# Performance work log

Measured on AMD Instinct MI355X. Metric: run time of the kernel, lower is better.

## Reference

```python
import jax, jax.numpy as jnp
import numpy as np

F, H, NSEQ, T, A, LP, LV = 256, 256, 64, 2048, 32, 512, 512
N = NSEQ * T


def setup_inputs() -> dict:
    key = jax.random.key(0)
    ks = jax.random.split(key, 24)
    p = lambda k, shape: jax.random.normal(k, shape, jnp.float32) * 0.05
    return {
        'features': jax.random.normal(ks[0], (N, F), jnp.float32),
        'episode_starts': (jax.random.uniform(ks[1], (N,)) < 0.005).astype(jnp.float32),
        'h_pi': jax.random.normal(ks[2], (1, NSEQ, H), jnp.float32),
        'c_pi': jax.random.normal(ks[3], (1, NSEQ, H), jnp.float32),
        'h_vf': jax.random.normal(ks[4], (1, NSEQ, H), jnp.float32),
        'c_vf': jax.random.normal(ks[5], (1, NSEQ, H), jnp.float32),
        'W_feat': p(ks[6], (4 * F, F)), 'b_feat': jnp.zeros((4 * F,), jnp.float32),
        'W_emb': p(ks[7], (H, F)), 'b_emb': jnp.zeros((H,), jnp.float32),
        'W_ih': p(ks[8], (4 * H, F)), 'W_hh': p(ks[9], (4 * H, H)),
        'b_ih': jnp.zeros((4 * H,), jnp.float32), 'b_hh': jnp.zeros((4 * H,), jnp.float32),
        'Wp1': p(ks[10], (LP, H + 3 * F)), 'bp1': jnp.zeros((LP,), jnp.float32),
        'Wp2': p(ks[11], (A, LP)), 'bp2': jnp.zeros((A,), jnp.float32),
        'Wv1': p(ks[12], (LV, H + 3 * F)), 'bv1': jnp.zeros((LV,), jnp.float32),
        'Wv2': p(ks[13], (1, LV)), 'bv2': jnp.zeros((1,), jnp.float32),
    }


def _lstm_masked_scan(feats, starts, h0, c0, W_ih, W_hh, b_ih, b_hh):
    # feats: (T, n_seq, F), starts: (T, n_seq); PyTorch gate order i,f,g,o
    xg = jnp.einsum('tnf,gf->tng', feats, W_ih) + b_ih  # precompute input gates

    def step(carry, xs):
        h, c = carry
        xg_t, s_t = xs
        m = (1.0 - s_t)[:, None]          # episode-reset mask
        h = h * m
        c = c * m
        g = xg_t + h @ W_hh.T + b_hh
        i, f, gg, o = jnp.split(g, 4, axis=-1)
        c = jax.nn.sigmoid(f) * c + jax.nn.sigmoid(i) * jnp.tanh(gg)
        h = jax.nn.sigmoid(o) * jnp.tanh(c)
        return (h, c), h

    (hT, cT), hs = jax.lax.scan(step, (h0, c0), (xg, starts))
    return hs, hT, cT


def reference(features, episode_starts, h_pi, c_pi, h_vf, c_vf,
              W_feat, b_feat, W_emb, b_emb, W_ih, W_hh, b_ih, b_hh,
              Wp1, bp1, Wp2, bp2, Wv1, bv1, Wv2, bv2):
    n_seq = h_vf.shape[1]
    feats = features.reshape(n_seq, -1, F).swapaxes(0, 1)      # (T, n_seq, F)
    starts = episode_starts.reshape(n_seq, -1).swapaxes(0, 1)  # (T, n_seq)

    feat4 = jnp.einsum('tnf,gf->tng', feats, W_feat) + b_feat  # (T, n_seq, 4F)
    f1 = feat4[..., : 3 * F]
    f1_flat = f1.swapaxes(0, 1).reshape(-1, 3 * F)             # (N, 3F)

    # actor branch: TempLSTM ignores its LSTM -> just Linear(F, H) on raw feats;
    # the loop branch feeds raw features_sequence (source behavior).
    out_pi = jnp.einsum('tnf,hf->tnh', feats, W_emb) + b_emb   # (T, n_seq, H)
    out_pi_flat = out_pi.swapaxes(0, 1).reshape(-1, H)

    # critic branch: masked LSTM recurrence with per-step episode resets
    hs, hT, cT = _lstm_masked_scan(feats, starts, h_vf[0], c_vf[0], W_ih, W_hh, b_ih, b_hh)
    hs_flat = hs.swapaxes(0, 1).reshape(-1, H)

    latent_pi = jnp.concatenate([f1_flat, out_pi_flat], axis=-1)
    latent_vf = jnp.concatenate([f1_flat, hs_flat], axis=-1)

    values = jax.nn.relu(latent_vf @ Wv1.T + bv1) @ Wv2.T + bv2      # (N, 1)
    logits = jax.nn.relu(latent_pi @ Wp1.T + bp1) @ Wp2.T + bp2      # (N, A)

    actions = jnp.argmax(logits, axis=-1)  # deterministic=True -> mode
    log_prob = jnp.take_along_axis(jax.nn.log_softmax(logits, axis=-1), actions[:, None], axis=1)[:, 0]

    # actor final state = h0 scaled by product of reset masks (loop semantics)
    mprod = jnp.prod(1.0 - starts, axis=0)[None, :, None]
    h_pi_f, c_pi_f = h_pi * mprod, c_pi * mprod
    return actions, values, log_prob, h_pi_f, c_pi_f, hT[None], cT[None]
```

## Files before the change

### kernel.cpp

```cpp
#include <hip/hip_runtime.h>
#include <stdint.h>
#include <math.h>

#define N_TOT 131072
#define TSEQ  2048
#define NSEQ  64
#define CS    128
#define NCH   16
#define PARTS 4

typedef unsigned long long u64;

__global__ __launch_bounds__(256)
void transpose_whh(const float* __restrict__ Whh, float* __restrict__ Wg)
{
    const int k = blockIdx.x;
    const int u = threadIdx.x;
#pragma unroll
    for (int g = 0; g < 4; ++g)
        Wg[(size_t)k * 1024 + u * 4 + g] = Whh[(size_t)(g * 256 + u) * 256 + k];
}

__global__ __launch_bounds__(256)
void gemm_xg(const float* __restrict__ A, const float* __restrict__ Wih,
             const float* __restrict__ bih, const float* __restrict__ bhh,
             float* __restrict__ xg, int base)
{
    __shared__ float As[16][136];
    __shared__ float Bs[16][136];
    const int t  = threadIdx.x;
    const int n0 = blockIdx.x * 128;
    const int seq = blockIdx.y;
    const size_t grow0 = (size_t)seq * TSEQ + base;
    const size_t lrow0 = (size_t)seq * CS;
    const int tx = t & 15, ty = t >> 4;

    float acc[8][8];
#pragma unroll
    for (int i = 0; i < 8; ++i)
#pragma unroll
        for (int j = 0; j < 8; ++j) acc[i][j] = 0.f;

    for (int kt = 0; kt < 256; kt += 16) {
#pragma unroll
        for (int jj = 0; jj < 2; ++jj) {
            int idx = t + 256 * jj;
            int m = idx >> 2, q = idx & 3;
            float4 a = *(const float4*)(A + (grow0 + m) * 256 + kt + q * 4);
            As[q * 4 + 0][m] = a.x; As[q * 4 + 1][m] = a.y;
            As[q * 4 + 2][m] = a.z; As[q * 4 + 3][m] = a.w;
            float4 b = *(const float4*)(Wih + (size_t)(n0 + m) * 256 + kt + q * 4);
            Bs[q * 4 + 0][m] = b.x; Bs[q * 4 + 1][m] = b.y;
            Bs[q * 4 + 2][m] = b.z; Bs[q * 4 + 3][m] = b.w;
        }
        __syncthreads();
#pragma unroll
        for (int k = 0; k < 16; ++k) {
            float4 a0 = *(const float4*)&As[k][ty * 8];
            float4 a1 = *(const float4*)&As[k][ty * 8 + 4];
            float4 b0 = *(const float4*)&Bs[k][tx * 8];
            float4 b1 = *(const float4*)&Bs[k][tx * 8 + 4];
            float av[8] = {a0.x, a0.y, a0.z, a0.w, a1.x, a1.y, a1.z, a1.w};
            float bv[8] = {b0.x, b0.y, b0.z, b0.w, b1.x, b1.y, b1.z, b1.w};
#pragma unroll
            for (int i = 0; i < 8; ++i)
#pragma unroll
                for (int j = 0; j < 8; ++j) acc[i][j] += av[i] * bv[j];
        }
        __syncthreads();
    }
#pragma unroll
    for (int i = 0; i < 8; ++i) {
        size_t lr = lrow0 + ty * 8 + i;
#pragma unroll
        for (int j = 0; j < 8; ++j) {
            int n = n0 + tx * 8 + j;
            int gate = n >> 8, u = n & 255;
            xg[lr * 1024 + u * 4 + gate] = acc[i][j] + bih[n] + bhh[n];
        }
    }
}

__device__ __forceinline__ void l2_store_u64(u64* p, u64 v)
{
    asm volatile("global_store_dwordx2 %0, %1, off"
                 :: "v"(p), "v"(v) : "memory");
}

__device__ __forceinline__ u64 l2_load_u64(const u64* p)
{
    u64 v;
    asm volatile("global_load_dwordx2 %0, %1, off sc0\n\t"
                 "s_waitcnt vmcnt(0)"
                 : "=v"(v) : "v"(p) : "memory");
    return v;
}

__global__ __launch_bounds__(1024)
void lstm4(const float* __restrict__ xg, const float* __restrict__ starts,
           const float* __restrict__ h0g, const float* __restrict__ c0g,
           float* __restrict__ hstate, float* __restrict__ cstate,
           const float* __restrict__ Wg,
           float* __restrict__ hs, float* __restrict__ hT,
           float* __restrict__ cT,
           u64* __restrict__ hx, u64* __restrict__ hx2,
           unsigned* __restrict__ fastState,
           int base, int fastflag)
{
    __shared__ float hmask[256];
    __shared__ float part[16][64][4];

    const int t    = threadIdx.x;
    const int bid  = blockIdx.x;
    const int slot = bid >> 3;
    const int seq  = (bid & 7) + 8 * (slot >> 2);
    const int p    = slot & 3;
    const int u    = t & 63;
    const int q    = t >> 6;

    float4 Wr[16];
#pragma unroll
    for (int kk = 0; kk < 16; ++kk)
        Wr[kk] = *(const float4*)(Wg + (size_t)(q * 16 + kk) * 1024 + (p * 64 + u) * 4);

    float c_reg = 0.f;
    if (t < 64) {
        const float* csrc = (base == 0) ? c0g : cstate;
        c_reg = csrc[(size_t)seq * 256 + p * 64 + t];
    }

    bool useFast = (fastflag != 0);
    if (useFast) {
        unsigned st = __hip_atomic_load(fastState, __ATOMIC_RELAXED,
                                        __HIP_MEMORY_SCOPE_AGENT);
        if (st != 0u) useFast = false;
    }

    for (int lt = 0; lt < CS; ++lt) {
        const int S = base + lt;
        const float m = 1.f - starts[(size_t)seq * TSEQ + S];

        float4 x4 = make_float4(0.f, 0.f, 0.f, 0.f);
        if (t < 64)
            x4 = *(const float4*)(xg + ((size_t)seq * CS + lt) * 1024 + (p * 64 + t) * 4);

        if (lt == 0) {
            if (t < 256) {
                const float* hsrc = (base == 0) ? h0g : hstate;
                hmask[t] = hsrc[(size_t)seq * 256 + t] * m;
            }
        } else {
            if (t < 256) {
                const size_t idx = (size_t)(S & 1) * (NSEQ * 256) + (size_t)seq * 256 + t;
                u64 w = 0;
                if (useFast) {
                    int tries = 0;
                    for (;;) {
                        w = l2_load_u64(&hx2[idx]);
                        if ((unsigned)(w >> 32) == (unsigned)S) break;
                        if (++tries > 768) {
                            useFast = false;
                            __hip_atomic_store(fastState, 1u, __ATOMIC_RELAXED,
                                               __HIP_MEMORY_SCOPE_AGENT);
                            break;
                        }
                    }
                }
                if (!useFast) {
                    unsigned spins = 0;
                    for (;;) {
                        w = __hip_atomic_load(&hx[idx], __ATOMIC_RELAXED,
                                              __HIP_MEMORY_SCOPE_AGENT);
                        if ((unsigned)(w >> 32) == (unsigned)S) break;
                        __builtin_amdgcn_s_sleep(1);
                        if (++spins > (1u << 18)) break;
                    }
                }
                hmask[t] = __uint_as_float((unsigned)w) * m;
            }
        }
        __syncthreads();

        const float* hp = &hmask[q * 16];
        float4 h0 = *(const float4*)(hp + 0);
        float4 h1 = *(const float4*)(hp + 4);
        float4 h2 = *(const float4*)(hp + 8);
        float4 h3 = *(const float4*)(hp + 12);
        float hv[16] = {h0.x,h0.y,h0.z,h0.w, h1.x,h1.y,h1.z,h1.w,
                        h2.x,h2.y,h2.z,h2.w, h3.x,h3.y,h3.z,h3.w};
        float a0 = 0.f, a1 = 0.f, a2 = 0.f, a3 = 0.f;
#pragma unroll
        for (int kk = 0; kk < 16; ++kk) {
            a0 += hv[kk] * Wr[kk].x;
            a1 += hv[kk] * Wr[kk].y;
            a2 += hv[kk] * Wr[kk].z;
            a3 += hv[kk] * Wr[kk].w;
        }
        *(float4*)&part[q][u][0] = make_float4(a0, a1, a2, a3);
        __syncthreads();

        if (t < 64) {
            float gi = 0.f, gf = 0.f, gg = 0.f, go = 0.f;
#pragma unroll
            for (int qq = 0; qq < 16; ++qq) {
                float4 pp = *(const float4*)&part[qq][t][0];
                gi += pp.x; gf += pp.y; gg += pp.z; go += pp.w;
            }
            gi += x4.x; gf += x4.y; gg += x4.z; go += x4.w;
            float c = c_reg * m;
            float si = 1.f / (1.f + expf(-gi));
            float sf = 1.f / (1.f + expf(-gf));
            float so = 1.f / (1.f + expf(-go));
            c = sf * c + si * tanhf(gg);
            float h = so * tanhf(c);
            c_reg = c;

            const int gu = p * 64 + t;
            const size_t widx = (size_t)((S + 1) & 1) * (NSEQ * 256)
                              + (size_t)seq * 256 + gu;
            const u64 pkt = ((u64)(unsigned)(S + 1) << 32)
                          | (u64)__float_as_uint(h);
            if (fastflag) l2_store_u64(&hx2[widx], pkt);
            __hip_atomic_store(&hx[widx], pkt,
                               __ATOMIC_RELAXED, __HIP_MEMORY_SCOPE_AGENT);
            hs[((size_t)seq * CS + lt) * 256 + gu] = h;
            if (lt == CS - 1) {
                cstate[(size_t)seq * 256 + gu] = c;
                hstate[(size_t)seq * 256 + gu] = h;
            }
            if (S == TSEQ - 1) {
                cT[(size_t)seq * 256 + gu] = c;
                hT[(size_t)seq * 256 + gu] = h;
            }
        }
    }
}

__global__ __launch_bounds__(256)
void gemm_latent(const float* __restrict__ A, const float* __restrict__ Wfeat,
                 const float* __restrict__ Wemb, const float* __restrict__ bfeat,
                 const float* __restrict__ bemb, float* __restrict__ lat, int base)
{
    __shared__ float As[16][136];
    __shared__ float Bs[16][136];
    const int t  = threadIdx.x;
    const int n0 = blockIdx.x * 128;
    const size_t lr0 = (size_t)blockIdx.y * 128;
    const size_t grow0 = (lr0 >> 7) * TSEQ + base;
    const int tx = t & 15, ty = t >> 4;

    double acc[8][8];
#pragma unroll
    for (int i = 0; i < 8; ++i)
#pragma unroll
        for (int j = 0; j < 8; ++j) acc[i][j] = 0.0;

    for (int kt = 0; kt < 256; kt += 16) {
#pragma unroll
        for (int jj = 0; jj < 2; ++jj) {
            int idx = t + 256 * jj;
            int m = idx >> 2, q = idx & 3;
            float4 a = *(const float4*)(A + (grow0 + m) * 256 + kt + q * 4);
            As[q * 4 + 0][m] = a.x; As[q * 4 + 1][m] = a.y;
            As[q * 4 + 2][m] = a.z; As[q * 4 + 3][m] = a.w;
            int n = n0 + m;
            const float* Brow = (n < 768) ? (Wfeat + (size_t)n * 256)
                                          : (Wemb + (size_t)(n - 768) * 256);
            float4 b = *(const float4*)(Brow + kt + q * 4);
            Bs[q * 4 + 0][m] = b.x; Bs[q * 4 + 1][m] = b.y;
            Bs[q * 4 + 2][m] = b.z; Bs[q * 4 + 3][m] = b.w;
        }
        __syncthreads();
        float p[8][8];
#pragma unroll
        for (int i = 0; i < 8; ++i)
#pragma unroll
            for (int j = 0; j < 8; ++j) p[i][j] = 0.f;
#pragma unroll
        for (int k = 0; k < 16; ++k) {
            float4 a0 = *(const float4*)&As[k][ty * 8];
            float4 a1 = *(const float4*)&As[k][ty * 8 + 4];
            float4 b0 = *(const float4*)&Bs[k][tx * 8];
            float4 b1 = *(const float4*)&Bs[k][tx * 8 + 4];
            float av[8] = {a0.x, a0.y, a0.z, a0.w, a1.x, a1.y, a1.z, a1.w};
            float bv[8] = {b0.x, b0.y, b0.z, b0.w, b1.x, b1.y, b1.z, b1.w};
#pragma unroll
            for (int i = 0; i < 8; ++i)
#pragma unroll
                for (int j = 0; j < 8; ++j) p[i][j] += av[i] * bv[j];
        }
#pragma unroll
        for (int i = 0; i < 8; ++i)
#pragma unroll
            for (int j = 0; j < 8; ++j) acc[i][j] += (double)p[i][j];
        __syncthreads();
    }
#pragma unroll
    for (int i = 0; i < 8; ++i) {
        size_t lr = lr0 + ty * 8 + i;
#pragma unroll
        for (int j = 0; j < 8; ++j) {
            int n = n0 + tx * 8 + j;
            float v = (float)acc[i][j];
            v += (n < 768) ? bfeat[n] : bemb[n - 768];
            lat[lr * 1024 + n] = v;
        }
    }
}

__global__ __launch_bounds__(256)
void gemm_h1p(const float* __restrict__ lat, const float* __restrict__ Wp1,
              const float* __restrict__ bp1, float* __restrict__ h1)
{
    __shared__ float As[16][136];
    __shared__ float Bs[16][136];
    const int t  = threadIdx.x;
    const int n0 = blockIdx.x * 128;
    const size_t lr0 = (size_t)blockIdx.y * 128;
    const int tx = t & 15, ty = t >> 4;

    double acc[8][8];
#pragma unroll
    for (int i = 0; i < 8; ++i)
#pragma unroll
        for (int j = 0; j < 8; ++j) acc[i][j] = 0.0;

    for (int kt = 0; kt < 1024; kt += 16) {
#pragma unroll
        for (int jj = 0; jj < 2; ++jj) {
            int idx = t + 256 * jj;
            int m = idx >> 2, q = idx & 3;
            float4 a = *(const float4*)(lat + (lr0 + m) * 1024 + kt + q * 4);
            As[q * 4 + 0][m] = a.x; As[q * 4 + 1][m] = a.y;
            As[q * 4 + 2][m] = a.z; As[q * 4 + 3][m] = a.w;
            float4 b = *(const float4*)(Wp1 + (size_t)(n0 + m) * 1024 + kt + q * 4);
            Bs[q * 4 + 0][m] = b.x; Bs[q * 4 + 1][m] = b.y;
            Bs[q * 4 + 2][m] = b.z; Bs[q * 4 + 3][m] = b.w;
        }
        __syncthreads();
        float p[8][8];
#pragma unroll
        for (int i = 0; i < 8; ++i)
#pragma unroll
            for (int j = 0; j < 8; ++j) p[i][j] = 0.f;
#pragma unroll
        for (int k = 0; k < 16; ++k) {
            float4 a0 = *(const float4*)&As[k][ty * 8];
            float4 a1 = *(const float4*)&As[k][ty * 8 + 4];
            float4 b0 = *(const float4*)&Bs[k][tx * 8];
            float4 b1 = *(const float4*)&Bs[k][tx * 8 + 4];
            float av[8] = {a0.x, a0.y, a0.z, a0.w, a1.x, a1.y, a1.z, a1.w};
            float bv[8] = {b0.x, b0.y, b0.z, b0.w, b1.x, b1.y, b1.z, b1.w};
#pragma unroll
            for (int i = 0; i < 8; ++i)
#pragma unroll
                for (int j = 0; j < 8; ++j) p[i][j] += av[i] * bv[j];
        }
#pragma unroll
        for (int i = 0; i < 8; ++i)
#pragma unroll
            for (int j = 0; j < 8; ++j) acc[i][j] += (double)p[i][j];
        __syncthreads();
    }
#pragma unroll
    for (int i = 0; i < 8; ++i) {
        size_t lr = lr0 + ty * 8 + i;
#pragma unroll
        for (int j = 0; j < 8; ++j) {
            int n = n0 + tx * 8 + j;
            float v = (float)acc[i][j] + bp1[n];
            h1[lr * 512 + n] = v > 0.f ? v : 0.f;
        }
    }
}

__global__ __launch_bounds__(256)
void gemm_h1v(const float* __restrict__ lat, const float* __restrict__ hs,
              const float* __restrict__ Wv1, const float* __restrict__ bv1,
              float* __restrict__ h1)
{
    __shared__ float As[16][136];
    __shared__ float Bs[16][136];
    const int t  = threadIdx.x;
    const int n0 = blockIdx.x * 128;
    const size_t lrow0 = (size_t)blockIdx.y * 128;
    const int tx = t & 15, ty = t >> 4;

    float acc[8][8];
#pragma unroll
    for (int i = 0; i < 8; ++i)
#pragma unroll
        for (int j = 0; j < 8; ++j) acc[i][j] = 0.f;

    for (int pass = 0; pass < 2; ++pass) {
        const float* A  = (pass == 0) ? lat : hs;
        const int lda   = (pass == 0) ? 1024 : 256;
        const int kmax  = (pass == 0) ? 768 : 256;
        const int boff  = (pass == 0) ? 0 : 768;
        for (int kt = 0; kt < kmax; kt += 16) {
#pragma unroll
            for (int jj = 0; jj < 2; ++jj) {
                int idx = t + 256 * jj;
                int m = idx >> 2, q = idx & 3;
                float4 a = *(const float4*)(A + (lrow0 + m) * lda + kt + q * 4);
                As[q * 4 + 0][m] = a.x; As[q * 4 + 1][m] = a.y;
                As[q * 4 + 2][m] = a.z; As[q * 4 + 3][m] = a.w;
                float4 b = *(const float4*)(Wv1 + (size_t)(n0 + m) * 1024 + boff + kt + q * 4);
                Bs[q * 4 + 0][m] = b.x; Bs[q * 4 + 1][m] = b.y;
                Bs[q * 4 + 2][m] = b.z; Bs[q * 4 + 3][m] = b.w;
            }
            __syncthreads();
#pragma unroll
            for (int k = 0; k < 16; ++k) {
                float4 a0 = *(const float4*)&As[k][ty * 8];
                float4 a1 = *(const float4*)&As[k][ty * 8 + 4];
                float4 b0 = *(const float4*)&Bs[k][tx * 8];
                float4 b1 = *(const float4*)&Bs[k][tx * 8 + 4];
                float av[8] = {a0.x, a0.y, a0.z, a0.w, a1.x, a1.y, a1.z, a1.w};
                float bv[8] = {b0.x, b0.y, b0.z, b0.w, b1.x, b1.y, b1.z, b1.w};
#pragma unroll
                for (int i = 0; i < 8; ++i)
#pragma unroll
                    for (int j = 0; j < 8; ++j) acc[i][j] += av[i] * bv[j];
            }
            __syncthreads();
        }
    }
#pragma unroll
    for (int i = 0; i < 8; ++i) {
        size_t lr = lrow0 + ty * 8 + i;
#pragma unroll
        for (int j = 0; j < 8; ++j) {
            int n = n0 + tx * 8 + j;
            float v = acc[i][j] + bv1[n];
            h1[lr * 512 + n] = v > 0.f ? v : 0.f;
        }
    }
}

__global__ __launch_bounds__(256)
void mask_kernel(const float* __restrict__ starts, const float* __restrict__ h_pi,
                 const float* __restrict__ c_pi,
                 float* __restrict__ o_hpi, float* __restrict__ o_cpi)
{
    __shared__ float red[256];
    const int n = blockIdx.x, t = threadIdx.x;
    float a = 0.f;
    for (int j = 0; j < 8; ++j)
        a = fmaxf(a, starts[(size_t)n * TSEQ + t * 8 + j]);
    red[t] = a; __syncthreads();
    for (int s = 128; s > 0; s >>= 1) {
        if (t < s) red[t] = fmaxf(red[t], red[t + s]);
        __syncthreads();
    }
    float m = (red[0] > 0.f) ? 0.f : 1.f;
    o_hpi[(size_t)n * 256 + t] = h_pi[(size_t)n * 256 + t] * m;
    o_cpi[(size_t)n * 256 + t] = c_pi[(size_t)n * 256 + t] * m;
}

__global__ __launch_bounds__(256)
void policy_finish(const float* __restrict__ h1p, const float* __restrict__ Wp2,
                   const float* __restrict__ bp2,
                   float* __restrict__ o_actions, float* __restrict__ o_logp,
                   int base)
{
    __shared__ float w2t[512 * 32];
    const int t = threadIdx.x;
    for (int j = 0; j < 64; ++j) {
        int idx = t + 256 * j;
        int k = idx >> 5, c = idx & 31;
        w2t[idx] = Wp2[(size_t)c * 512 + k];
    }
    __syncthreads();

    const int c = t & 31;
    size_t lr = (size_t)blockIdx.x * 8 + (t >> 5);
    size_t grow = (lr >> 7) * TSEQ + base + (lr & 127);
    const float* hrow = h1p + lr * 512;
    double s = 0.0;
    for (int k = 0; k < 512; k += 4) {
        float4 h4 = *(const float4*)(hrow + k);
        s += (double)h4.x * (double)w2t[(k + 0) * 32 + c];
        s += (double)h4.y * (double)w2t[(k + 1) * 32 + c];
        s += (double)h4.z * (double)w2t[(k + 2) * 32 + c];
        s += (double)h4.w * (double)w2t[(k + 3) * 32 + c];
    }
    double logit = s + (double)bp2[c];

    double mv = logit; int mi = c;
#pragma unroll
    for (int off = 16; off >= 1; off >>= 1) {
        double ov = __shfl_xor(mv, off, 32);
        int    oi = __shfl_xor(mi, off, 32);
        if (ov > mv || (ov == mv && oi < mi)) { mv = ov; mi = oi; }
    }
    double se = exp(logit - mv);
#pragma unroll
    for (int off = 16; off >= 1; off >>= 1) se += __shfl_xor(se, off, 32);

    if (c == 0) {
        o_actions[grow] = (float)mi;
        o_logp[grow]    = (float)(-log(se));
    }
}

__global__ __launch_bounds__(256)
void value_finish(const float* __restrict__ h1v, const float* __restrict__ Wv2,
                  const float* __restrict__ bv2, float* __restrict__ o_values,
                  int base)
{
    __shared__ float wv[512];
    const int t = threadIdx.x;
    wv[t] = Wv2[t]; wv[t + 256] = Wv2[t + 256];
    __syncthreads();
    const int q = t & 3;
    size_t lr = (size_t)blockIdx.x * 64 + (t >> 2);
    size_t grow = (lr >> 7) * TSEQ + base + (lr & 127);
    const float* hrow = h1v + lr * 512;
    float s = 0.f;
    for (int k = q * 128; k < q * 128 + 128; k += 4) {
        float4 h4 = *(const float4*)(hrow + k);
        float4 w4 = *(const float4*)&wv[k];
        s += h4.x * w4.x + h4.y * w4.y + h4.z * w4.z + h4.w * w4.w;
    }
    s += __shfl_xor(s, 1, 4);
    s += __shfl_xor(s, 2, 4);
    if (q == 0) o_values[grow] = s + bv2[0];
}

extern "C" void kernel_launch(void* const* d_in, const int* in_sizes, int n_in,
                              void* d_out, int out_size, void* d_ws, size_t ws_size,
                              hipStream_t stream)
{
    const float* features = (const float*)d_in[0];
    const float* starts   = (const float*)d_in[1];
    const float* h_pi     = (const float*)d_in[2];
    const float* c_pi     = (const float*)d_in[3];
    const float* h_vf     = (const float*)d_in[4];
    const float* c_vf     = (const float*)d_in[5];
    const float* W_feat   = (const float*)d_in[6];
    const float* b_feat   = (const float*)d_in[7];
    const float* W_emb    = (const float*)d_in[8];
    const float* b_emb    = (const float*)d_in[9];
    const float* W_ih     = (const float*)d_in[10];
    const float* W_hh     = (const float*)d_in[11];
    const float* b_ih     = (const float*)d_in[12];
    const float* b_hh     = (const float*)d_in[13];
    const float* Wp1      = (const float*)d_in[14];
    const float* bp1      = (const float*)d_in[15];
    const float* Wp2      = (const float*)d_in[16];
    const float* bp2      = (const float*)d_in[17];
    const float* Wv1      = (const float*)d_in[18];
    const float* bv1      = (const float*)d_in[19];
    const float* Wv2      = (const float*)d_in[20];
    const float* bv2      = (const float*)d_in[21];

    float* out = (float*)d_out;
    float* o_actions = out;
    float* o_values  = out + N_TOT;
    float* o_logp    = out + 2 * (size_t)N_TOT;
    float* o_hpi     = out + 3 * (size_t)N_TOT;
    float* o_cpi     = o_hpi + NSEQ * 256;
    float* o_hT      = o_cpi + NSEQ * 256;
    float* o_cT      = o_hT  + NSEQ * 256;

    char* ws = (char*)d_ws;
    const size_t MB = 1024 * 1024;
    float* xg_c  = (float*)(ws);
    float* lat_c = (float*)(ws + 32 * MB);
    float* hs_c  = (float*)(ws + 64 * MB);
    float* h1_c  = (float*)(ws + 72 * MB);
    float* Wg    = (float*)(ws + 88 * MB);
    float* hstate = (float*)(ws + 89 * MB);
    float* cstate = (float*)(ws + 89 * MB + 65536);
    u64*   hx     = (u64*)  (ws + 89 * MB + 131072);
    u64*   hx2    = (u64*)  (ws + 89 * MB + 393216);
    unsigned* fastState = (unsigned*)(ws + 89 * MB + 655360);

    const int fastflag = (ws_size >= 89 * MB + 656 * 1024) ? 1 : 0;
    u64* hx2_eff = fastflag ? hx2 : hx;
    unsigned* fs_eff = fastflag ? fastState : (unsigned*)hx;

    transpose_whh<<<256, 256, 0, stream>>>(W_hh, Wg);

    mask_kernel<<<NSEQ, 256, 0, stream>>>(starts, h_pi, c_pi, o_hpi, o_cpi);

    for (int c = 0; c < NCH; ++c) {
        const int base = c * CS;

        gemm_xg<<<dim3(8, NSEQ), 256, 0, stream>>>(features, W_ih, b_ih, b_hh,
                                                   xg_c, base);
        lstm4<<<NSEQ * PARTS, 1024, 0, stream>>>(xg_c, starts, h_vf, c_vf,
                                                 hstate, cstate, Wg,
                                                 hs_c, o_hT, o_cT, hx, hx2_eff,
                                                 fs_eff, base, fastflag);

        gemm_latent<<<dim3(8, 64), 256, 0, stream>>>(
            features, W_feat, W_emb, b_feat, b_emb, lat_c, base);

        gemm_h1p<<<dim3(4, 64), 256, 0, stream>>>(lat_c, Wp1, bp1, h1_c);
        policy_finish<<<1024, 256, 0, stream>>>(h1_c, Wp2, bp2,
                                                o_actions, o_logp, base);

        gemm_h1v<<<dim3(4, 64), 256, 0, stream>>>(lat_c, hs_c, Wv1, bv1, h1_c);
        value_finish<<<128, 256, 0, stream>>>(h1_c, Wv2, bv2, o_values, base);
    }
}
```

Before: 16.65 ms.

## Co-schedule policy hidden-layer GEMM inside LSTM kernel launch to overlap recurrence

Merges the LSTM recurrence and the policy first-layer GEMM into one launch: blocks 0-255 run the latency-bound recurrence while blocks 256-511 compute the h1p GEMM as four 64x64 sub-tiles per 1024-thread block. gemm_latent is moved ahead so its output is ready. The goal is to fill idle compute units during the serial recurrence. The risk is that GEMM blocks compete for CUs, cache and memory bandwidth with the spin-waiting LSTM blocks, and that all 256 LSTM blocks may no longer be co-resident, which the spin waits depend on.

```diff
diff --git a/kernel.cpp b/kernel.cpp
--- a/kernel.cpp
+++ b/kernel.cpp
@@ -97,140 +97,206 @@
 }
 
 __global__ __launch_bounds__(1024)
-void lstm4(const float* __restrict__ xg, const float* __restrict__ starts,
-           const float* __restrict__ h0g, const float* __restrict__ c0g,
-           float* __restrict__ hstate, float* __restrict__ cstate,
-           const float* __restrict__ Wg,
-           float* __restrict__ hs, float* __restrict__ hT,
-           float* __restrict__ cT,
-           u64* __restrict__ hx, u64* __restrict__ hx2,
-           unsigned* __restrict__ fastState,
-           int base, int fastflag)
-{
-    __shared__ float hmask[256];
-    __shared__ float part[16][64][4];
-
-    const int t    = threadIdx.x;
-    const int bid  = blockIdx.x;
-    const int slot = bid >> 3;
-    const int seq  = (bid & 7) + 8 * (slot >> 2);
-    const int p    = slot & 3;
-    const int u    = t & 63;
-    const int q    = t >> 6;
-
-    float4 Wr[16];
-#pragma unroll
-    for (int kk = 0; kk < 16; ++kk)
-        Wr[kk] = *(const float4*)(Wg + (size_t)(q * 16 + kk) * 1024 + (p * 64 + u) * 4);
-
-    float c_reg = 0.f;
-    if (t < 64) {
-        const float* csrc = (base == 0) ? c0g : cstate;
-        c_reg = csrc[(size_t)seq * 256 + p * 64 + t];
-    }
-
-    bool useFast = (fastflag != 0);
-    if (useFast) {
-        unsigned st = __hip_atomic_load(fastState, __ATOMIC_RELAXED,
-                                        __HIP_MEMORY_SCOPE_AGENT);
-        if (st != 0u) useFast = false;
-    }
-
-    for (int lt = 0; lt < CS; ++lt) {
-        const int S = base + lt;
-        const float m = 1.f - starts[(size_t)seq * TSEQ + S];
-
-        float4 x4 = make_float4(0.f, 0.f, 0.f, 0.f);
-        if (t < 64)
-            x4 = *(const float4*)(xg + ((size_t)seq * CS + lt) * 1024 + (p * 64 + t) * 4);
-
-        if (lt == 0) {
-            if (t < 256) {
-                const float* hsrc = (base == 0) ? h0g : hstate;
-                hmask[t] = hsrc[(size_t)seq * 256 + t] * m;
-            }
-        } else {
-            if (t < 256) {
-                const size_t idx = (size_t)(S & 1) * (NSEQ * 256) + (size_t)seq * 256 + t;
-                u64 w = 0;
-                if (useFast) {
-                    int tries = 0;
-                    for (;;) {
-                        w = l2_load_u64(&hx2[idx]);
-                        if ((unsigned)(w >> 32) == (unsigned)S) break;
-                        if (++tries > 768) {
-                            useFast = false;
-                            __hip_atomic_store(fastState, 1u, __ATOMIC_RELAXED,
-                                               __HIP_MEMORY_SCOPE_AGENT);
-                            break;
+void lstm4_h1p(const float* __restrict__ xg, const float* __restrict__ starts,
+               const float* __restrict__ h0g, const float* __restrict__ c0g,
+               float* __restrict__ hstate, float* __restrict__ cstate,
+               const float* __restrict__ Wg,
+               float* __restrict__ hs, float* __restrict__ hT,
+               float* __restrict__ cT,
+               u64* __restrict__ hx, u64* __restrict__ hx2,
+               unsigned* __restrict__ fastState,
+               const float* __restrict__ lat, const float* __restrict__ Wp1,
+               const float* __restrict__ bp1, float* __restrict__ h1,
+               int base, int fastflag)
+{
+    __shared__ float smem[9216];
+
+    const int t   = threadIdx.x;
+    const int bid = blockIdx.x;
+
+    if (bid < 256) {
+        float* hmask = smem;
+        float* part  = smem + 256;
+
+        const int slot = bid >> 3;
+        const int seq  = (bid & 7) + 8 * (slot >> 2);
+        const int p    = slot & 3;
+        const int u    = t & 63;
+        const int q    = t >> 6;
+
+        float4 Wr[16];
+#pragma unroll
+        for (int kk = 0; kk < 16; ++kk)
+            Wr[kk] = *(const float4*)(Wg + (size_t)(q * 16 + kk) * 1024 + (p * 64 + u) * 4);
+
+        float c_reg = 0.f;
+        if (t < 64) {
+            const float* csrc = (base == 0) ? c0g : cstate;
+            c_reg = csrc[(size_t)seq * 256 + p * 64 + t];
+        }
+
+        bool useFast = (fastflag != 0);
+        if (useFast) {
+            unsigned st = __hip_atomic_load(fastState, __ATOMIC_RELAXED,
+                                            __HIP_MEMORY_SCOPE_AGENT);
+            if (st != 0u) useFast = false;
+        }
+
+        for (int lt = 0; lt < CS; ++lt) {
+            const int S = base + lt;
+            const float m = 1.f - starts[(size_t)seq * TSEQ + S];
+
+            float4 x4 = make_float4(0.f, 0.f, 0.f, 0.f);
+            if (t < 64)
+                x4 = *(const float4*)(xg + ((size_t)seq * CS + lt) * 1024 + (p * 64 + t) * 4);
+
+            if (lt == 0) {
+                if (t < 256) {
+                    const float* hsrc = (base == 0) ? h0g : hstate;
+                    hmask[t] = hsrc[(size_t)seq * 256 + t] * m;
+                }
+            } else {
+                if (t < 256) {
+                    const size_t idx = (size_t)(S & 1) * (NSEQ * 256) + (size_t)seq * 256 + t;
+                    u64 w = 0;
+                    if (useFast) {
+                        int tries = 0;
+                        for (;;) {
+                            w = l2_load_u64(&hx2[idx]);
+                            if ((unsigned)(w >> 32) == (unsigned)S) break;
+                            if (++tries > 768) {
+                                useFast = false;
+                                __hip_atomic_store(fastState, 1u, __ATOMIC_RELAXED,
+                                                   __HIP_MEMORY_SCOPE_AGENT);
+                                break;
+                            }
                         }
                     }
+                    if (!useFast) {
+                        unsigned spins = 0;
+                        for (;;) {
+                            w = __hip_atomic_load(&hx[idx], __ATOMIC_RELAXED,
+                                                  __HIP_MEMORY_SCOPE_AGENT);
+                            if ((unsigned)(w >> 32) == (unsigned)S) break;
+                            __builtin_amdgcn_s_sleep(1);
+                            if (++spins > (1u << 18)) break;
+                        }
+                    }
+                    hmask[t] = __uint_as_float((unsigned)w) * m;
                 }
-                if (!useFast) {
-                    unsigned spins = 0;
-                    for (;;) {
-                        w = __hip_atomic_load(&hx[idx], __ATOMIC_RELAXED,
-                                              __HIP_MEMORY_SCOPE_AGENT);
-                        if ((unsigned)(w >> 32) == (unsigned)S) break;
-                        __builtin_amdgcn_s_sleep(1);
-                        if (++spins > (1u << 18)) break;
-                    }
+            }
+            __syncthreads();
+
+            const float* hp = &hmask[q * 16];
+            float4 h0 = *(const float4*)(hp + 0);
+            float4 h1v_ = *(const float4*)(hp + 4);
+            float4 h2 = *(const float4*)(hp + 8);
+            float4 h3 = *(const float4*)(hp + 12);
+            float hv[16] = {h0.x,h0.y,h0.z,h0.w, h1v_.x,h1v_.y,h1v_.z,h1v_.w,
+                            h2.x,h2.y,h2.z,h2.w, h3.x,h3.y,h3.z,h3.w};
+            float a0 = 0.f, a1 = 0.f, a2 = 0.f, a3 = 0.f;
+#pragma unroll
+            for (int kk = 0; kk < 16; ++kk) {
+                a0 += hv[kk] * Wr[kk].x;
+                a1 += hv[kk] * Wr[kk].y;
+                a2 += hv[kk] * Wr[kk].z;
+                a3 += hv[kk] * Wr[kk].w;
+            }
+            *(float4*)&part[(q * 64 + u) * 4] = make_float4(a0, a1, a2, a3);
+            __syncthreads();
+
+            if (t < 64) {
+                float gi = 0.f, gf = 0.f, gg = 0.f, go = 0.f;
+#pragma unroll
+                for (int qq = 0; qq < 16; ++qq) {
+                    float4 pp = *(const float4*)&part[(qq * 64 + t) * 4];
+                    gi += pp.x; gf += pp.y; gg += pp.z; go += pp.w;
                 }
-                hmask[t] = __uint_as_float((unsigned)w) * m;
-            }
-        }
-        __syncthreads();
-
-        const float* hp = &hmask[q * 16];
-        float4 h0 = *(const float4*)(hp + 0);
-        float4 h1 = *(const float4*)(hp + 4);
-        float4 h2 = *(const float4*)(hp + 8);
-        float4 h3 = *(const float4*)(hp + 12);
-        float hv[16] = {h0.x,h0.y,h0.z,h0.w, h1.x,h1.y,h1.z,h1.w,
-                        h2.x,h2.y,h2.z,h2.w, h3.x,h3.y,h3.z,h3.w};
-        float a0 = 0.f, a1 = 0.f, a2 = 0.f, a3 = 0.f;
-#pragma unroll
-        for (int kk = 0; kk < 16; ++kk) {
-            a0 += hv[kk] * Wr[kk].x;
-            a1 += hv[kk] * Wr[kk].y;
-            a2 += hv[kk] * Wr[kk].z;
-            a3 += hv[kk] * Wr[kk].w;
-        }
-        *(float4*)&part[q][u][0] = make_float4(a0, a1, a2, a3);
-        __syncthreads();
-
-        if (t < 64) {
-            float gi = 0.f, gf = 0.f, gg = 0.f, go = 0.f;
-#pragma unroll
-            for (int qq = 0; qq < 16; ++qq) {
-                float4 pp = *(const float4*)&part[qq][t][0];
-                gi += pp.x; gf += pp.y; gg += pp.z; go += pp.w;
-            }
-            gi += x4.x; gf += x4.y; gg += x4.z; go += x4.w;
-            float c = c_reg * m;
-            float si = 1.f / (1.f + expf(-gi));
-            float sf = 1.f / (1.f + expf(-gf));
-            float so = 1.f / (1.f + expf(-go));
-            c = sf * c + si * tanhf(gg);
-            float h = so * tanhf(c);
-            c_reg = c;
-
-            const int gu = p * 64 + t;
-            const size_t widx = (size_t)((S + 1) & 1) * (NSEQ * 256)
-                              + (size_t)seq * 256 + gu;
-            const u64 pkt = ((u64)(unsigned)(S + 1) << 32)
-                          | (u64)__float_as_uint(h);
-            if (fastflag) l2_store_u64(&hx2[widx], pkt);
-            __hip_atomic_store(&hx[widx], pkt,
-                               __ATOMIC_RELAXED, __HIP_MEMORY_SCOPE_AGENT);
-            hs[((size_t)seq * CS + lt) * 256 + gu] = h;
-            if (lt == CS - 1) {
-                cstate[(size_t)seq * 256 + gu] = c;
-                hstate[(size_t)seq * 256 + gu] = h;
-            }
-            if (S == TSEQ - 1) {
-                cT[(size_t)seq * 256 + gu] = c;
-                hT[(size_t)seq * 256 + gu] = h;
+                gi += x4.x; gf += x4.y; gg += x4.z; go += x4.w;
+                float c = c_reg * m;
+                float si = 1.f / (1.f + expf(-gi));
+                float sf = 1.f / (1.f + expf(-gf));
+                float so = 1.f / (1.f + expf(-go));
+                c = sf * c + si * tanhf(gg);
+                float h = so * tanhf(c);
+                c_reg = c;
+
+                const int gu = p * 64 + t;
+                const size_t widx = (size_t)((S + 1) & 1) * (NSEQ * 256)
+                                  + (size_t)seq * 256 + gu;
+                const u64 pkt = ((u64)(unsigned)(S + 1) << 32)
+                              | (u64)__float_as_uint(h);
+                if (fastflag) l2_store_u64(&hx2[widx], pkt);
+                __hip_atomic_store(&hx[widx], pkt,
+                                   __ATOMIC_RELAXED, __HIP_MEMORY_SCOPE_AGENT);
+                hs[((size_t)seq * CS + lt) * 256 + gu] = h;
+                if (lt == CS - 1) {
+                    cstate[(size_t)seq * 256 + gu] = c;
+                    hstate[(size_t)seq * 256 + gu] = h;
+                }
+                if (S == TSEQ - 1) {
+                    cT[(size_t)seq * 256 + gu] = c;
+                    hT[(size_t)seq * 256 + gu] = h;
+                }
+            }
+        }
+    } else {
+        const int s    = t >> 8;
+        const int t2   = t & 255;
+        const int tile = (bid - 256) * 4 + s;
+        const int n0   = (tile & 7) * 64;
+        const size_t lr0 = (size_t)(tile >> 3) * 64;
+        float* As = smem + s * 2304;
+        float* Bs = As + 1152;
+        const int tx = t2 & 15, ty = t2 >> 4;
+
+        double acc[4][4];
+#pragma unroll
+        for (int i = 0; i < 4; ++i)
+#pragma unroll
+            for (int j = 0; j < 4; ++j) acc[i][j] = 0.0;
+
+        for (int kt = 0; kt < 1024; kt += 16) {
+            {
+                int m = t2 >> 2, q = t2 & 3;
+                float4 a = *(const float4*)(lat + (lr0 + m) * 1024 + kt + q * 4);
+                As[(q * 4 + 0) * 72 + m] = a.x; As[(q * 4 + 1) * 72 + m] = a.y;
+                As[(q * 4 + 2) * 72 + m] = a.z; As[(q * 4 + 3) * 72 + m] = a.w;
+                float4 b = *(const float4*)(Wp1 + (size_t)(n0 + m) * 1024 + kt + q * 4);
+                Bs[(q * 4 + 0) * 72 + m] = b.x; Bs[(q * 4 + 1) * 72 + m] = b.y;
+                Bs[(q * 4 + 2) * 72 + m] = b.z; Bs[(q * 4 + 3) * 72 + m] = b.w;
+            }
+            __syncthreads();
+            float p[4][4];
+#pragma unroll
+            for (int i = 0; i < 4; ++i)
+#pragma unroll
+                for (int j = 0; j < 4; ++j) p[i][j] = 0.f;
+#pragma unroll
+            for (int k = 0; k < 16; ++k) {
+                float4 a0 = *(const float4*)&As[k * 72 + ty * 4];
+                float4 b0 = *(const float4*)&Bs[k * 72 + tx * 4];
+                float av[4] = {a0.x, a0.y, a0.z, a0.w};
+                float bv[4] = {b0.x, b0.y, b0.z, b0.w};
+#pragma unroll
+                for (int i = 0; i < 4; ++i)
+#pragma unroll
+                    for (int j = 0; j < 4; ++j) p[i][j] += av[i] * bv[j];
+            }
+#pragma unroll
+            for (int i = 0; i < 4; ++i)
+#pragma unroll
+                for (int j = 0; j < 4; ++j) acc[i][j] += (double)p[i][j];
+            __syncthreads();
+        }
+#pragma unroll
+        for (int i = 0; i < 4; ++i) {
+            size_t lr = lr0 + ty * 4 + i;
+#pragma unroll
+            for (int j = 0; j < 4; ++j) {
+                int n = n0 + tx * 4 + j;
+                float v = (float)acc[i][j] + bp1[n];
+                h1[lr * 512 + n] = v > 0.f ? v : 0.f;
             }
         }
     }
@@ -304,72 +370,6 @@
             float v = (float)acc[i][j];
             v += (n < 768) ? bfeat[n] : bemb[n - 768];
             lat[lr * 1024 + n] = v;
-        }
-    }
-}
-
-__global__ __launch_bounds__(256)
-void gemm_h1p(const float* __restrict__ lat, const float* __restrict__ Wp1,
-              const float* __restrict__ bp1, float* __restrict__ h1)
-{
-    __shared__ float As[16][136];
-    __shared__ float Bs[16][136];
-    const int t  = threadIdx.x;
-    const int n0 = blockIdx.x * 128;
-    const size_t lr0 = (size_t)blockIdx.y * 128;
-    const int tx = t & 15, ty = t >> 4;
-
-    double acc[8][8];
-#pragma unroll
-    for (int i = 0; i < 8; ++i)
-#pragma unroll
-        for (int j = 0; j < 8; ++j) acc[i][j] = 0.0;
-
-    for (int kt = 0; kt < 1024; kt += 16) {
-#pragma unroll
-        for (int jj = 0; jj < 2; ++jj) {
-            int idx = t + 256 * jj;
-            int m = idx >> 2, q = idx & 3;
-            float4 a = *(const float4*)(lat + (lr0 + m) * 1024 + kt + q * 4);
-            As[q * 4 + 0][m] = a.x; As[q * 4 + 1][m] = a.y;
-            As[q * 4 + 2][m] = a.z; As[q * 4 + 3][m] = a.w;
-            float4 b = *(const float4*)(Wp1 + (size_t)(n0 + m) * 1024 + kt + q * 4);
-            Bs[q * 4 + 0][m] = b.x; Bs[q * 4 + 1][m] = b.y;
-            Bs[q * 4 + 2][m] = b.z; Bs[q * 4 + 3][m] = b.w;
-        }
-        __syncthreads();
-        float p[8][8];
-#pragma unroll
-        for (int i = 0; i < 8; ++i)
-#pragma unroll
-            for (int j = 0; j < 8; ++j) p[i][j] = 0.f;
-#pragma unroll
-        for (int k = 0; k < 16; ++k) {
-            float4 a0 = *(const float4*)&As[k][ty * 8];
-            float4 a1 = *(const float4*)&As[k][ty * 8 + 4];
-            float4 b0 = *(const float4*)&Bs[k][tx * 8];
-            float4 b1 = *(const float4*)&Bs[k][tx * 8 + 4];
-            float av[8] = {a0.x, a0.y, a0.z, a0.w, a1.x, a1.y, a1.z, a1.w};
-            float bv[8] = {b0.x, b0.y, b0.z, b0.w, b1.x, b1.y, b1.z, b1.w};
-#pragma unroll
-            for (int i = 0; i < 8; ++i)
-#pragma unroll
-                for (int j = 0; j < 8; ++j) p[i][j] += av[i] * bv[j];
-        }
-#pragma unroll
-        for (int i = 0; i < 8; ++i)
-#pragma unroll
-            for (int j = 0; j < 8; ++j) acc[i][j] += (double)p[i][j];
-        __syncthreads();
-    }
-#pragma unroll
-    for (int i = 0; i < 8; ++i) {
-        size_t lr = lr0 + ty * 8 + i;
-#pragma unroll
-        for (int j = 0; j < 8; ++j) {
-            int n = n0 + tx * 8 + j;
-            float v = (float)acc[i][j] + bp1[n];
-            h1[lr * 512 + n] = v > 0.f ? v : 0.f;
         }
     }
 }
@@ -590,15 +590,16 @@
 
         gemm_xg<<<dim3(8, NSEQ), 256, 0, stream>>>(features, W_ih, b_ih, b_hh,
                                                    xg_c, base);
-        lstm4<<<NSEQ * PARTS, 1024, 0, stream>>>(xg_c, starts, h_vf, c_vf,
-                                                 hstate, cstate, Wg,
-                                                 hs_c, o_hT, o_cT, hx, hx2_eff,
-                                                 fs_eff, base, fastflag);
-
         gemm_latent<<<dim3(8, 64), 256, 0, stream>>>(
             features, W_feat, W_emb, b_feat, b_emb, lat_c, base);
 
-        gemm_h1p<<<dim3(4, 64), 256, 0, stream>>>(lat_c, Wp1, bp1, h1_c);
+        lstm4_h1p<<<512, 1024, 0, stream>>>(xg_c, starts, h_vf, c_vf,
+                                            hstate, cstate, Wg,
+                                            hs_c, o_hT, o_cT, hx, hx2_eff,
+                                            fs_eff,
+                                            lat_c, Wp1, bp1, h1_c,
+                                            base, fastflag);
+
         policy_finish<<<1024, 256, 0, stream>>>(h1_c, Wp2, bp2,
                                                 o_actions, o_logp, base);
 
```

Measured after the change: 14.74 ms. 1.13x faster.
